# Optimization experiments

Measured on AMD Instinct MI355X. Metric: run time of the kernel, lower is better.

## Reference

```python
import jax, jax.numpy as jnp
import numpy as np

N = 40000      # nodes
E = 640000     # edges (avg degree 16)
ND = 128       # node_dim
ED = 64        # edge_dim
LN_EPS = 1e-5


def setup_inputs() -> dict:
    key = jax.random.key(0)
    ks = jax.random.split(key, 16)
    s = lambda k, shape, fan_in: jax.random.normal(k, shape, dtype=jnp.float32) * (1.0 / np.sqrt(fan_in))
    return {
        "node_features": jax.random.normal(ks[0], (N, ND), dtype=jnp.float32),
        "edge_indices": jax.random.randint(ks[1], (2, E), 0, N, dtype=jnp.int32),
        "edge_features": jax.random.normal(ks[2], (E, ED), dtype=jnp.float32),
        # message_mlp: Linear(2*ND+ED -> ND), LayerNorm(ND), ReLU, Linear(ND -> ND)
        "W1": s(ks[3], (2 * ND + ED, ND), 2 * ND + ED),
        "b1": jnp.zeros((ND,), jnp.float32),
        "ln_g": jnp.ones((ND,), jnp.float32),
        "ln_b": jnp.zeros((ND,), jnp.float32),
        "W2": s(ks[4], (ND, ND), ND),
        "b2": jnp.zeros((ND,), jnp.float32),
        # edge_gate: Linear(ED -> 1) + Sigmoid
        "gate_w": s(ks[5], (ED, 1), ED),
        "gate_b": jnp.zeros((1,), jnp.float32),
        # GRUCell(ND, ND): weight_ih [3*ND, ND], weight_hh [3*ND, ND] (gates r, z, n)
        "W_ih": s(ks[6], (3 * ND, ND), ND),
        "b_ih": jnp.zeros((3 * ND,), jnp.float32),
        "W_hh": s(ks[7], (3 * ND, ND), ND),
        "b_hh": jnp.zeros((3 * ND,), jnp.float32),
    }


def reference(node_features, edge_indices, edge_features, W1, b1, ln_g, ln_b,
              W2, b2, gate_w, gate_b, W_ih, b_ih, W_hh, b_hh):
    src, dst = edge_indices[0], edge_indices[1]
    # gather src/dst node features and concat with edge features -> [E, 2*ND+ED]
    edge_inputs = jnp.concatenate(
        [node_features[src], node_features[dst], edge_features], axis=1)
    # message MLP: Linear -> LayerNorm -> ReLU -> Linear
    h = edge_inputs @ W1 + b1
    mu = jnp.mean(h, axis=-1, keepdims=True)
    var = jnp.var(h, axis=-1, keepdims=True)
    h = (h - mu) * jax.lax.rsqrt(var + LN_EPS) * ln_g + ln_b
    h = jax.nn.relu(h)
    messages = h @ W2 + b2                                   # [E, ND]
    # sigmoid edge gate from raw edge features
    gate = jax.nn.sigmoid(edge_features @ gate_w + gate_b)   # [E, 1]
    messages = messages * gate
    # scatter-add into destination nodes
    agg = jax.ops.segment_sum(messages, dst, num_segments=node_features.shape[0])
    # GRUCell(input=agg, hidden=node_features), torch gate order: r, z, n
    gi = agg @ W_ih.T + b_ih
    gh = node_features @ W_hh.T + b_hh
    i_r, i_z, i_n = jnp.split(gi, 3, axis=1)
    h_r, h_z, h_n = jnp.split(gh, 3, axis=1)
    r = jax.nn.sigmoid(i_r + h_r)
    z = jax.nn.sigmoid(i_z + h_z)
    n = jnp.tanh(i_n + r * h_n)
    return (1.0 - z) * n + z * node_features
```

## Files before the change

kernel.cpp:

```cpp
#include <hip/hip_runtime.h>
#include <math.h>

#define ND 128
#define ED 64
#define LN_EPS 1e-5f
#define TE 64
#define SXH 328
#define GSH 136
#define GSF 132

typedef _Float16 f16;
typedef __attribute__((ext_vector_type(8))) _Float16 f16x8;
typedef __attribute__((ext_vector_type(4))) _Float16 f16x4;
typedef __attribute__((ext_vector_type(4))) float f32x4;

__device__ __forceinline__ float sigmoidf_(float x) { return 1.f / (1.f + expf(-x)); }

__global__ void convert_kernel(const float* __restrict__ W1, const float* __restrict__ W2,
                               const float* __restrict__ Wih, const float* __restrict__ Whh,
                               f16* __restrict__ W1f, f16* __restrict__ W2f,
                               f16* __restrict__ Wihf, f16* __restrict__ Whhf)
{
    int idx = blockIdx.x * 256 + threadIdx.x;
    if (idx < 40960) {
        int n = idx / 320, k = idx - n * 320;
        W1f[idx] = (f16)W1[k * 128 + n];
    } else if (idx < 57344) {
        int i2 = idx - 40960; int n = i2 >> 7, k = i2 & 127;
        W2f[i2] = (f16)W2[k * 128 + n];
    } else if (idx < 106496) {
        int i3 = idx - 57344;  Wihf[i3] = (f16)Wih[i3];
    } else if (idx < 155648) {
        int i4 = idx - 106496; Whhf[i4] = (f16)Whh[i4];
    }
}

__global__ void hist_kernel(const int* __restrict__ eidx, int* __restrict__ cnt, int E) {
    int i = blockIdx.x * 256 + threadIdx.x;
    if (i < E) atomicAdd(&cnt[eidx[E + i]], 1);
}

__global__ __launch_bounds__(1024)
void scan_kernel(const int* __restrict__ cnt, int* __restrict__ woff, int N) {
    __shared__ int part[1024];
    const int t = threadIdx.x;
    const int CH = 40;
    int base = t * CH;
    int s = 0;
    for (int i = 0; i < CH; ++i) { int idx = base + i; if (idx < N) s += cnt[idx]; }
    part[t] = s;
    __syncthreads();
    for (int d = 1; d < 1024; d <<= 1) {
        int v = (t >= d) ? part[t - d] : 0;
        __syncthreads();
        part[t] += v;
        __syncthreads();
    }
    int run = (t == 0) ? 0 : part[t - 1];
    for (int i = 0; i < CH; ++i) {
        int idx = base + i;
        if (idx < N) { woff[idx] = run; run += cnt[idx]; }
    }
}

__global__ void scatter_kernel(const int* __restrict__ eidx, int* __restrict__ woff,
                               int* __restrict__ perm, int E) {
    int i = blockIdx.x * 256 + threadIdx.x;
    if (i < E) {
        int p = atomicAdd(&woff[eidx[E + i]], 1);
        perm[p] = i;
    }
}

__global__ __launch_bounds__(256, 3)
void edge_kernel(const float* __restrict__ nf, const int* __restrict__ eidx,
                 const float* __restrict__ ef, const int* __restrict__ perm,
                 const f16* __restrict__ W1f, const float* __restrict__ b1,
                 const float* __restrict__ ln_g, const float* __restrict__ ln_b,
                 const f16* __restrict__ W2f, const float* __restrict__ b2,
                 const float* __restrict__ gate_w, const float* __restrict__ gate_b,
                 float* __restrict__ agg, int E)
{
    __shared__ f16   sxh[TE * SXH];
    __shared__ float sred[TE * 8];
    __shared__ float spart[TE][4];
    __shared__ float sg[TE];
    __shared__ int   se_s[TE], ssrc_s[TE], sdst_s[TE];

    const int tid  = threadIdx.x;
    const int lane = tid & 63;
    const int w    = __builtin_amdgcn_readfirstlane(tid >> 6);
    const int cb   = 32 * w;
    const int c    = lane & 15;
    const int quad = lane >> 4;
    const int e0   = blockIdx.x * TE;

    if (tid < TE) {
        int e = perm[e0 + tid];
        se_s[tid]   = e;
        ssrc_s[tid] = eidx[e];
        sdst_s[tid] = eidx[E + e];
    }
    __syncthreads();

    {
        const int r = tid >> 2, q = tid & 3;
        const float* srow = nf + (size_t)ssrc_s[r] * ND;
        const float* drow = nf + (size_t)sdst_s[r] * ND;
        const float* erow = ef + (size_t)se_s[r] * ED;
        f16* dp = sxh + r * SXH;
        #pragma unroll
        for (int i = 0; i < 8; ++i) {
            int ec = (q + 4 * i) * 4;
            float4 v = *(const float4*)(srow + ec);
            f16x4 h4; h4[0] = (f16)v.x; h4[1] = (f16)v.y; h4[2] = (f16)v.z; h4[3] = (f16)v.w;
            *(f16x4*)(dp + ec) = h4;
        }
        #pragma unroll
        for (int i = 0; i < 8; ++i) {
            int ec = (q + 4 * i) * 4;
            float4 v = *(const float4*)(drow + ec);
            f16x4 h4; h4[0] = (f16)v.x; h4[1] = (f16)v.y; h4[2] = (f16)v.z; h4[3] = (f16)v.w;
            *(f16x4*)(dp + 128 + ec) = h4;
        }
        #pragma unroll
        for (int i = 0; i < 4; ++i) {
            int ec = (q + 4 * i) * 4;
            float4 v = *(const float4*)(erow + ec);
            f16x4 h4; h4[0] = (f16)v.x; h4[1] = (f16)v.y; h4[2] = (f16)v.z; h4[3] = (f16)v.w;
            *(f16x4*)(dp + 256 + ec) = h4;
        }
    }
    __syncthreads();

    {
        const int grow = tid >> 2, gq = tid & 3;
        const f16* ep = sxh + grow * SXH + 256 + gq * 16;
        f16x8 e0v = *(const f16x8*)ep;
        f16x8 e1v = *(const f16x8*)(ep + 8);
        float p = 0.f;
        #pragma unroll
        for (int j = 0; j < 8; ++j) {
            p = fmaf((float)e0v[j], gate_w[gq * 16 + j], p);
            p = fmaf((float)e1v[j], gate_w[gq * 16 + 8 + j], p);
        }
        spart[grow][gq] = p;
    }
    __syncthreads();
    if (tid < TE)
        sg[tid] = sigmoidf_(spart[tid][0] + spart[tid][1] + spart[tid][2] + spart[tid][3] + gate_b[0]);

    f32x4 acc[4][2];
    #pragma unroll
    for (int mt = 0; mt < 4; ++mt)
        #pragma unroll
        for (int nt = 0; nt < 2; ++nt) acc[mt][nt] = (f32x4){0.f, 0.f, 0.f, 0.f};

    #pragma unroll
    for (int ks = 0; ks < 10; ++ks) {
        f16x8 b0 = *(const f16x8*)(W1f + (cb + c) * 320 + ks * 32 + quad * 8);
        f16x8 b1v = *(const f16x8*)(W1f + (cb + 16 + c) * 320 + ks * 32 + quad * 8);
        #pragma unroll
        for (int mt = 0; mt < 4; ++mt) {
            f16x8 a = *(const f16x8*)(sxh + (16 * mt + c) * SXH + ks * 32 + quad * 8);
            acc[mt][0] = __builtin_amdgcn_mfma_f32_16x16x32_f16(a, b0,  acc[mt][0], 0, 0, 0);
            acc[mt][1] = __builtin_amdgcn_mfma_f32_16x16x32_f16(a, b1v, acc[mt][1], 0, 0, 0);
        }
    }

    float b1c[2], gvc[2], bvc[2], b2c[2];
    #pragma unroll
    for (int nt = 0; nt < 2; ++nt) {
        int col = cb + nt * 16 + c;
        b1c[nt] = b1[col]; gvc[nt] = ln_g[col]; bvc[nt] = ln_b[col]; b2c[nt] = b2[col];
    }
    #pragma unroll
    for (int mt = 0; mt < 4; ++mt) {
        float p1[4] = {0, 0, 0, 0}, p2[4] = {0, 0, 0, 0};
        #pragma unroll
        for (int nt = 0; nt < 2; ++nt)
            #pragma unroll
            for (int r = 0; r < 4; ++r) {
                float vv = acc[mt][nt][r] + b1c[nt];
                acc[mt][nt][r] = vv;
                p1[r] += vv; p2[r] += vv * vv;
            }
        #pragma unroll
        for (int m = 1; m < 16; m <<= 1)
            #pragma unroll
            for (int r = 0; r < 4; ++r) {
                p1[r] += __shfl_xor(p1[r], m);
                p2[r] += __shfl_xor(p2[r], m);
            }
        if (c == 0) {
            #pragma unroll
            for (int r = 0; r < 4; ++r) {
                int row = 16 * mt + 4 * quad + r;
                sred[row * 8 + 2 * w + 0] = p1[r];
                sred[row * 8 + 2 * w + 1] = p2[r];
            }
        }
    }
    __syncthreads();

    #pragma unroll
    for (int mt = 0; mt < 4; ++mt)
        #pragma unroll
        for (int r = 0; r < 4; ++r) {
            int row = 16 * mt + 4 * quad + r;
            f32x4 lo = *(const f32x4*)(sred + row * 8);
            f32x4 hi = *(const f32x4*)(sred + row * 8 + 4);
            float t1 = lo[0] + lo[2] + hi[0] + hi[2];
            float t2 = lo[1] + lo[3] + hi[1] + hi[3];
            float mu = t1 * (1.f / 128.f);
            float var = t2 * (1.f / 128.f) - mu * mu;
            float rs = rsqrtf(var + LN_EPS);
            #pragma unroll
            for (int nt = 0; nt < 2; ++nt) {
                float vv = (acc[mt][nt][r] - mu) * rs * gvc[nt] + bvc[nt];
                vv = vv > 0.f ? vv : 0.f;
                sxh[row * SXH + cb + nt * 16 + c] = (f16)vv;
            }
        }
    __syncthreads();

    f32x4 acc2[4][2];
    #pragma unroll
    for (int mt = 0; mt < 4; ++mt)
        #pragma unroll
        for (int nt = 0; nt < 2; ++nt) acc2[mt][nt] = (f32x4){0.f, 0.f, 0.f, 0.f};
    #pragma unroll
    for (int ks = 0; ks < 4; ++ks) {
        f16x8 b0 = *(const f16x8*)(W2f + (cb + c) * 128 + ks * 32 + quad * 8);
        f16x8 b1v = *(const f16x8*)(W2f + (cb + 16 + c) * 128 + ks * 32 + quad * 8);
        #pragma unroll
        for (int mt = 0; mt < 4; ++mt) {
            f16x8 a = *(const f16x8*)(sxh + (16 * mt + c) * SXH + ks * 32 + quad * 8);
            acc2[mt][0] = __builtin_amdgcn_mfma_f32_16x16x32_f16(a, b0,  acc2[mt][0], 0, 0, 0);
            acc2[mt][1] = __builtin_amdgcn_mfma_f32_16x16x32_f16(a, b1v, acc2[mt][1], 0, 0, 0);
        }
    }
    __syncthreads();

    float* smsg = (float*)sxh;
    #pragma unroll
    for (int mt = 0; mt < 4; ++mt)
        #pragma unroll
        for (int r = 0; r < 4; ++r) {
            int row = 16 * mt + 4 * quad + r;
            float gr = sg[row];
            #pragma unroll
            for (int nt = 0; nt < 2; ++nt)
                smsg[row * 164 + cb + nt * 16 + c] = (acc2[mt][nt][r] + b2c[nt]) * gr;
        }
    __syncthreads();

    if (tid < 128) {
        const int col = tid;
        float run = smsg[col];
        int prev = sdst_s[0];
        for (int r = 1; r < TE; ++r) {
            int d = sdst_s[r];
            float v = smsg[r * 164 + col];
            if (d == prev) run += v;
            else {
                atomicAdd(agg + (size_t)prev * ND + col, run);
                run = v; prev = d;
            }
        }
        atomicAdd(agg + (size_t)prev * ND + col, run);
    }
}

__global__ __launch_bounds__(256, 2)
void gru_kernel(const float* __restrict__ agg, const float* __restrict__ nf,
                const f16* __restrict__ Wihf, const float* __restrict__ b_ih,
                const f16* __restrict__ Whhf, const float* __restrict__ b_hh,
                float* __restrict__ out)
{
    __shared__ f16   sa[32 * GSH];
    __shared__ f16   sh[32 * GSH];
    __shared__ float shf[32 * GSF];

    const int tid  = threadIdx.x;
    const int lane = tid & 63;
    const int w    = __builtin_amdgcn_readfirstlane(tid >> 6);
    const int c    = lane & 15;
    const int quad = lane >> 4;
    const int n0   = blockIdx.x * 32;

    {
        const int r = tid >> 3, q = tid & 7;
        const float* arow = agg + (size_t)(n0 + r) * ND;
        const float* hrow = nf  + (size_t)(n0 + r) * ND;
        #pragma unroll
        for (int i = 0; i < 4; ++i) {
            int ec = (q + 8 * i) * 4;
            float4 va = *(const float4*)(arow + ec);
            f16x4 ha; ha[0] = (f16)va.x; ha[1] = (f16)va.y; ha[2] = (f16)va.z; ha[3] = (f16)va.w;
            *(f16x4*)(sa + r * GSH + ec) = ha;
            float4 vh = *(const float4*)(hrow + ec);
            f16x4 hh; hh[0] = (f16)vh.x; hh[1] = (f16)vh.y; hh[2] = (f16)vh.z; hh[3] = (f16)vh.w;
            *(f16x4*)(sh + r * GSH + ec) = hh;
            *(float4*)(shf + r * GSF + ec) = vh;
        }
    }
    __syncthreads();

    f32x4 aI[2][6], aH[2][6];
    #pragma unroll
    for (int mt = 0; mt < 2; ++mt)
        #pragma unroll
        for (int j = 0; j < 6; ++j) {
            aI[mt][j] = (f32x4){0.f, 0.f, 0.f, 0.f};
            aH[mt][j] = (f32x4){0.f, 0.f, 0.f, 0.f};
        }

    #pragma unroll
    for (int ks = 0; ks < 4; ++ks) {
        f16x8 fa[2], fh[2];
        #pragma unroll
        for (int mt = 0; mt < 2; ++mt) {
            fa[mt] = *(const f16x8*)(sa + (16 * mt + c) * GSH + ks * 32 + quad * 8);
            fh[mt] = *(const f16x8*)(sh + (16 * mt + c) * GSH + ks * 32 + quad * 8);
        }
        #pragma unroll
        for (int gg = 0; gg < 3; ++gg)
            #pragma unroll
            for (int nt = 0; nt < 2; ++nt) {
                int coln = gg * 128 + 32 * w + nt * 16 + c;
                f16x8 bI = *(const f16x8*)(Wihf + coln * 128 + ks * 32 + quad * 8);
                f16x8 bH = *(const f16x8*)(Whhf + coln * 128 + ks * 32 + quad * 8);
                #pragma unroll
                for (int mt = 0; mt < 2; ++mt) {
                    int j = gg * 2 + nt;
                    aI[mt][j] = __builtin_amdgcn_mfma_f32_16x16x32_f16(fa[mt], bI, aI[mt][j], 0, 0, 0);
                    aH[mt][j] = __builtin_amdgcn_mfma_f32_16x16x32_f16(fh[mt], bH, aH[mt][j], 0, 0, 0);
                }
            }
    }

    #pragma unroll
    for (int nt = 0; nt < 2; ++nt) {
        int col = 32 * w + nt * 16 + c;
        float bir = b_ih[col], biz = b_ih[128 + col], bin = b_ih[256 + col];
        float bhr = b_hh[col], bhz = b_hh[128 + col], bhn = b_hh[256 + col];
        #pragma unroll
        for (int mt = 0; mt < 2; ++mt)
            #pragma unroll
            for (int r = 0; r < 4; ++r) {
                int row = 16 * mt + 4 * quad + r;
                float rr = sigmoidf_(aI[mt][0 + nt][r] + bir + aH[mt][0 + nt][r] + bhr);
                float zz = sigmoidf_(aI[mt][2 + nt][r] + biz + aH[mt][2 + nt][r] + bhz);
                float nn = tanhf(aI[mt][4 + nt][r] + bin + rr * (aH[mt][4 + nt][r] + bhn));
                float hp = shf[row * GSF + col];
                out[(size_t)(n0 + row) * ND + col] = (1.f - zz) * nn + zz * hp;
            }
    }
}

extern "C" void kernel_launch(void* const* d_in, const int* in_sizes, int n_in,
                              void* d_out, int out_size, void* d_ws, size_t ws_size,
                              hipStream_t stream) {
    const float* nf     = (const float*)d_in[0];
    const int*   eidx   = (const int*)  d_in[1];
    const float* ef     = (const float*)d_in[2];
    const float* W1     = (const float*)d_in[3];
    const float* b1     = (const float*)d_in[4];
    const float* ln_g   = (const float*)d_in[5];
    const float* ln_b   = (const float*)d_in[6];
    const float* W2     = (const float*)d_in[7];
    const float* b2     = (const float*)d_in[8];
    const float* gate_w = (const float*)d_in[9];
    const float* gate_b = (const float*)d_in[10];
    const float* W_ih   = (const float*)d_in[11];
    const float* b_ih   = (const float*)d_in[12];
    const float* W_hh   = (const float*)d_in[13];
    const float* b_hh   = (const float*)d_in[14];
    float* out = (float*)d_out;

    const int N = in_sizes[0] / ND;
    const int E = in_sizes[1] / 2;

    char* ws = (char*)d_ws;
    float* agg = (float*)ws;          ws += (size_t)N * ND * 4;
    f16* W1f  = (f16*)ws;             ws += 40960 * 2;
    f16* W2f  = (f16*)ws;             ws += 16384 * 2;
    f16* Wihf = (f16*)ws;             ws += 49152 * 2;
    f16* Whhf = (f16*)ws;             ws += 49152 * 2;
    int* cnt  = (int*)ws;             ws += 40960 * 4;
    int* woff = (int*)ws;             ws += 40960 * 4;
    int* perm = (int*)ws;             ws += (size_t)E * 4;

    hipMemsetAsync(agg, 0, (size_t)N * ND * 4, stream);
    hipMemsetAsync(cnt, 0, (size_t)N * 4, stream);
    convert_kernel<<<608, 256, 0, stream>>>(W1, W2, W_ih, W_hh, W1f, W2f, Wihf, Whhf);
    hist_kernel<<<(E + 255) / 256, 256, 0, stream>>>(eidx, cnt, E);
    scan_kernel<<<1, 1024, 0, stream>>>(cnt, woff, N);
    scatter_kernel<<<(E + 255) / 256, 256, 0, stream>>>(eidx, woff, perm, E);
    edge_kernel<<<E / TE, 256, 0, stream>>>(nf, eidx, ef, perm, W1f, b1, ln_g, ln_b,
                                            W2f, b2, gate_w, gate_b, agg, E);
    gru_kernel<<<N / 32, 256, 0, stream>>>(agg, nf, Wihf, b_ih, Whhf, b_hh, out);
}
```

Before: 650.9 us.

## Pre-convert node features to fp16, fuse gate dot, parallelize segmented scatter

```diff
diff --git a/kernel.cpp b/kernel.cpp
--- a/kernel.cpp
+++ b/kernel.cpp
@@ -35,6 +35,18 @@
     }
 }
 
+__global__ void nf16_kernel(const float* __restrict__ nf, f16* __restrict__ nf16, int n8) {
+    int i = blockIdx.x * 256 + threadIdx.x;
+    if (i < n8) {
+        float4 a = ((const float4*)nf)[2 * i];
+        float4 b = ((const float4*)nf)[2 * i + 1];
+        f16x8 h;
+        h[0] = (f16)a.x; h[1] = (f16)a.y; h[2] = (f16)a.z; h[3] = (f16)a.w;
+        h[4] = (f16)b.x; h[5] = (f16)b.y; h[6] = (f16)b.z; h[7] = (f16)b.w;
+        ((f16x8*)nf16)[i] = h;
+    }
+}
+
 __global__ void hist_kernel(const int* __restrict__ eidx, int* __restrict__ cnt, int E) {
     int i = blockIdx.x * 256 + threadIdx.x;
     if (i < E) atomicAdd(&cnt[eidx[E + i]], 1);
@@ -73,7 +85,7 @@
 }
 
 __global__ __launch_bounds__(256, 3)
-void edge_kernel(const float* __restrict__ nf, const int* __restrict__ eidx,
+void edge_kernel(const f16* __restrict__ nf16, const int* __restrict__ eidx,
                  const float* __restrict__ ef, const int* __restrict__ perm,
                  const f16* __restrict__ W1f, const float* __restrict__ b1,
                  const float* __restrict__ ln_g, const float* __restrict__ ln_b,
@@ -105,48 +117,31 @@
 
     {
         const int r = tid >> 2, q = tid & 3;
-        const float* srow = nf + (size_t)ssrc_s[r] * ND;
-        const float* drow = nf + (size_t)sdst_s[r] * ND;
+        const f16*   srow = nf16 + (size_t)ssrc_s[r] * ND;
+        const f16*   drow = nf16 + (size_t)sdst_s[r] * ND;
         const float* erow = ef + (size_t)se_s[r] * ED;
         f16* dp = sxh + r * SXH;
         #pragma unroll
-        for (int i = 0; i < 8; ++i) {
-            int ec = (q + 4 * i) * 4;
-            float4 v = *(const float4*)(srow + ec);
-            f16x4 h4; h4[0] = (f16)v.x; h4[1] = (f16)v.y; h4[2] = (f16)v.z; h4[3] = (f16)v.w;
-            *(f16x4*)(dp + ec) = h4;
-        }
-        #pragma unroll
-        for (int i = 0; i < 8; ++i) {
-            int ec = (q + 4 * i) * 4;
-            float4 v = *(const float4*)(drow + ec);
-            f16x4 h4; h4[0] = (f16)v.x; h4[1] = (f16)v.y; h4[2] = (f16)v.z; h4[3] = (f16)v.w;
-            *(f16x4*)(dp + 128 + ec) = h4;
-        }
+        for (int i = 0; i < 4; ++i) {
+            int ch = (q + 4 * i) * 8;
+            *(f16x8*)(dp + ch)       = *(const f16x8*)(srow + ch);
+            *(f16x8*)(dp + 128 + ch) = *(const f16x8*)(drow + ch);
+        }
+        float gp = 0.f;
         #pragma unroll
         for (int i = 0; i < 4; ++i) {
             int ec = (q + 4 * i) * 4;
             float4 v = *(const float4*)(erow + ec);
             f16x4 h4; h4[0] = (f16)v.x; h4[1] = (f16)v.y; h4[2] = (f16)v.z; h4[3] = (f16)v.w;
             *(f16x4*)(dp + 256 + ec) = h4;
-        }
-    }
-    __syncthreads();
-
-    {
-        const int grow = tid >> 2, gq = tid & 3;
-        const f16* ep = sxh + grow * SXH + 256 + gq * 16;
-        f16x8 e0v = *(const f16x8*)ep;
-        f16x8 e1v = *(const f16x8*)(ep + 8);
-        float p = 0.f;
-        #pragma unroll
-        for (int j = 0; j < 8; ++j) {
-            p = fmaf((float)e0v[j], gate_w[gq * 16 + j], p);
-            p = fmaf((float)e1v[j], gate_w[gq * 16 + 8 + j], p);
-        }
-        spart[grow][gq] = p;
-    }
-    __syncthreads();
+            const float* gw = gate_w + ec;
+            gp = fmaf(v.x, gw[0], gp); gp = fmaf(v.y, gw[1], gp);
+            gp = fmaf(v.z, gw[2], gp); gp = fmaf(v.w, gw[3], gp);
+        }
+        spart[r][q] = gp;
+    }
+    __syncthreads();
+
     if (tid < TE)
         sg[tid] = sigmoidf_(spart[tid][0] + spart[tid][1] + spart[tid][2] + spart[tid][3] + gate_b[0]);
 
@@ -255,20 +250,26 @@
         }
     __syncthreads();
 
-    if (tid < 128) {
-        const int col = tid;
-        float run = smsg[col];
-        int prev = sdst_s[0];
-        for (int r = 1; r < TE; ++r) {
-            int d = sdst_s[r];
-            float v = smsg[r * 164 + col];
-            if (d == prev) run += v;
+    {
+        const int rbase = 16 * w;
+        const float* sm = smsg + rbase * 164;
+        float run0 = sm[lane];
+        float run1 = sm[64 + lane];
+        int prev = __builtin_amdgcn_readfirstlane(sdst_s[rbase]);
+        #pragma unroll
+        for (int r = 1; r < 16; ++r) {
+            int d = __builtin_amdgcn_readfirstlane(sdst_s[rbase + r]);
+            float v0 = sm[r * 164 + lane];
+            float v1 = sm[r * 164 + 64 + lane];
+            if (d == prev) { run0 += v0; run1 += v1; }
             else {
-                atomicAdd(agg + (size_t)prev * ND + col, run);
-                run = v; prev = d;
-            }
-        }
-        atomicAdd(agg + (size_t)prev * ND + col, run);
+                atomicAdd(agg + (size_t)prev * ND + lane,      run0);
+                atomicAdd(agg + (size_t)prev * ND + 64 + lane, run1);
+                run0 = v0; run1 = v1; prev = d;
+            }
+        }
+        atomicAdd(agg + (size_t)prev * ND + lane,      run0);
+        atomicAdd(agg + (size_t)prev * ND + 64 + lane, run1);
     }
 }
 
@@ -384,6 +385,7 @@
 
     char* ws = (char*)d_ws;
     float* agg = (float*)ws;          ws += (size_t)N * ND * 4;
+    f16* nf16 = (f16*)ws;             ws += (size_t)N * ND * 2;
     f16* W1f  = (f16*)ws;             ws += 40960 * 2;
     f16* W2f  = (f16*)ws;             ws += 16384 * 2;
     f16* Wihf = (f16*)ws;             ws += 49152 * 2;
@@ -395,10 +397,12 @@
     hipMemsetAsync(agg, 0, (size_t)N * ND * 4, stream);
     hipMemsetAsync(cnt, 0, (size_t)N * 4, stream);
     convert_kernel<<<608, 256, 0, stream>>>(W1, W2, W_ih, W_hh, W1f, W2f, Wihf, Whhf);
+    const int n8 = N * ND / 8;
+    nf16_kernel<<<(n8 + 255) / 256, 256, 0, stream>>>(nf, nf16, n8);
     hist_kernel<<<(E + 255) / 256, 256, 0, stream>>>(eidx, cnt, E);
     scan_kernel<<<1, 1024, 0, stream>>>(cnt, woff, N);
     scatter_kernel<<<(E + 255) / 256, 256, 0, stream>>>(eidx, woff, perm, E);
-    edge_kernel<<<E / TE, 256, 0, stream>>>(nf, eidx, ef, perm, W1f, b1, ln_g, ln_b,
+    edge_kernel<<<E / TE, 256, 0, stream>>>(nf16, eidx, ef, perm, W1f, b1, ln_g, ln_b,
                                             W2f, b2, gate_w, gate_b, agg, E);
     gru_kernel<<<N / 32, 256, 0, stream>>>(agg, nf, Wihf, b_ih, Whhf, b_hh, out);
 }
```

Result: faster. 611.6 us (-6.0%).
